# Kernel tuning notes

Measured on AMD Instinct MI355X. Metric: run time of the kernel, lower is better.

The kernel has to match this reference:

```python
import jax, jax.numpy as jnp
import numpy as np

QK_I2_S = 128  # elements per packed block (32 bytes -> 128 2-bit weights)


def unpack_weights_simd(packed):
    """Unpack SIMD block-interleaved 2-bit ternary weights.

    packed: (M, K//4) int values in [0, 256). Per 32-byte block, byte j holds
    weights at offsets j+0 (bits 6:7), j+32 (bits 4:5), j+64 (bits 2:3), j+96 (bits 0:1).
    Returns float32 (M, K) with values in {-1, 0, 1, 2}-1 = {-1,0,1,2}? (2-bit code minus 1).
    """
    M, Kp = packed.shape
    nb = Kp // 32                      # number of 128-element blocks
    p = packed.reshape(M, nb, 32)
    shifts = jnp.array([6, 4, 2, 0], dtype=jnp.int32)
    # (M, nb, 4, 32): axis 2 indexes the offset group {0,32,64,96}
    w = ((p[:, :, None, :] >> shifts[None, None, :, None]) & 3).astype(jnp.float32) - 1.0
    return w.reshape(M, nb * QK_I2_S)  # (M, K)


def quantize_activations_i8(x):
    """Per-token symmetric int8 quantization (absmax -> [-128, 127])."""
    absmax = jnp.max(jnp.abs(x), axis=-1, keepdims=True)
    q_scale = 127.0 / jnp.clip(absmax, 1e-5, None)   # x_i8 = round(x * q_scale)
    x_i8 = jnp.clip(jnp.round(x * q_scale), -128.0, 127.0)
    act_scale = 1.0 / q_scale                         # dequant scale = absmax/127
    return x_i8, act_scale


def setup_inputs() -> dict:
    key = jax.random.key(0)
    k1, k2, k3 = jax.random.split(key, 3)
    x = jax.random.normal(k1, (2, 2048, 4096), dtype=jnp.float32)
    weight = jax.random.randint(k2, (12288, 1024), 0, 256, dtype=jnp.int32)
    weight_scale = jax.random.uniform(k3, (1,), dtype=jnp.float32, minval=0.01, maxval=0.1)
    return {"x": x, "weight": weight, "weight_scale": weight_scale}


def reference(x, weight, weight_scale):
    orig_shape = x.shape[:-1]
    K = x.shape[-1]
    x_flat = x.reshape(-1, K).astype(jnp.float32)
    x_i8, act_scale = quantize_activations_i8(x_flat)      # (N,K), (N,1)
    W = unpack_weights_simd(weight)                         # (M,K) ternary-coded floats
    # bitnet_gemm: int8 activations x ternary weights, fused weight scale
    out = jnp.einsum('nk,mk->nm', x_i8, W) * weight_scale[0]
    out = (out * act_scale).astype(x.dtype)                 # dequantize activations
    return out.reshape(*orig_shape, -1)
```

## Files before the change

kernel.cpp:

```cpp
#include <hip/hip_runtime.h>

#define K_DIM 4096
#define M_DIM 12288
#define KW 1024
#define NT_K 32
#define BM 256
#define BN 256
#define GN 16
#define GM 48

typedef __attribute__((ext_vector_type(4))) int i32x4;
typedef __attribute__((ext_vector_type(16))) int i32x16;
typedef __attribute__((ext_vector_type(4))) unsigned int u32x4;
typedef __attribute__((ext_vector_type(4))) float f32x4;

__device__ __forceinline__ int quant1(float v, float qs) {
  float r = rintf(v * qs);
  r = fminf(127.f, fmaxf(-128.f, r));
  return (int)r;
}

__device__ __forceinline__ unsigned int unp(unsigned int uv) {
  return ((uv >> 6) | (uv << 4) | (uv << 14) | (uv << 24)) & 0x03030303u;
}

__global__ __launch_bounds__(256) void aux_kernel(const float* __restrict__ x,
                                                  const int* __restrict__ wp,
                                                  u32x4* __restrict__ xq2,
                                                  u32x4* __restrict__ wu2,
                                                  float2* __restrict__ scales) {
  __shared__ float redf[4];
  __shared__ int redi[4];
  __shared__ u32x4 ldsT[32][9];
  const int t = threadIdx.x;

  if (blockIdx.x < 4096) {
    const int n = blockIdx.x;
    const f32x4* __restrict__ row4 = (const f32x4*)(x + (size_t)n * K_DIM);

    float am = 0.f;
#pragma unroll
    for (int p = 0; p < 4; ++p) {
      f32x4 v = row4[t + 256 * p];
      am = fmaxf(am, fmaxf(fmaxf(fabsf(v[0]), fabsf(v[1])), fmaxf(fabsf(v[2]), fabsf(v[3]))));
    }
#pragma unroll
    for (int off = 32; off; off >>= 1) am = fmaxf(am, __shfl_xor(am, off, 64));
    const int wave = t >> 6, lane = t & 63;
    if (lane == 0) redf[wave] = am;
    __syncthreads();
    am = fmaxf(fmaxf(redf[0], redf[1]), fmaxf(redf[2], redf[3]));
    const float clipped = fmaxf(am, 1e-5f);
    const float qs = 127.0f / clipped;

    f32x4 v[4];
#pragma unroll
    for (int s = 0; s < 4; ++s) v[s] = row4[(t >> 3) * 32 + (t & 7) + 8 * s];
    unsigned int wds[4];
    int rsum = 0;
#pragma unroll
    for (int m = 0; m < 4; ++m) {
      const int q0 = quant1(v[0][m], qs);
      const int q1 = quant1(v[1][m], qs);
      const int q2 = quant1(v[2][m], qs);
      const int q3 = quant1(v[3][m], qs);
      rsum += q0 + q1 + q2 + q3;
      wds[m] = (unsigned int)(q0 & 255) | ((unsigned int)(q1 & 255) << 8) |
               ((unsigned int)(q2 & 255) << 16) | ((unsigned int)(q3 & 255) << 24);
    }
    xq2[(size_t)t * 4096 + n] = (u32x4){wds[0], wds[1], wds[2], wds[3]};

#pragma unroll
    for (int off = 32; off; off >>= 1) rsum += __shfl_xor(rsum, off, 64);
    if (lane == 0) redi[wave] = rsum;
    __syncthreads();
    if (t == 0)
      scales[n] = make_float2(clipped * (1.0f / 127.0f),
                              (float)(redi[0] + redi[1] + redi[2] + redi[3]));
  } else {
    const int bid = blockIdx.x - 4096;
    const int mt = bid >> 5, kb = bid & 31;
    const int m0 = mt * 256;
    const i32x4* __restrict__ in4 = (const i32x4*)wp;
#pragma unroll 2
    for (int it = 0; it < 8; ++it) {
      const int m = m0 + it * 32 + (t >> 3);
      const i32x4 vv = in4[(size_t)m * 256 + kb * 8 + (t & 7)];
      ldsT[t >> 3][t & 7] = (u32x4){unp((unsigned int)vv[0]), unp((unsigned int)vv[1]),
                                    unp((unsigned int)vv[2]), unp((unsigned int)vv[3])};
      __syncthreads();
      wu2[(size_t)(kb * 8 + (t >> 5)) * M_DIM + m0 + it * 32 + (t & 31)] = ldsT[t & 31][t >> 5];
      __syncthreads();
    }
  }
}

#define DSR(dst, addr, off) \
  asm volatile("ds_read_b128 %0, %1 offset:" #off : "=v"(dst) : "v"(addr))
#define LGKM(n) asm volatile("s_waitcnt lgkmcnt(" #n ")")

#define RD_KS0(s) { DSR(af[s][0], aA, 0);     DSR(af[s][1], aA, 512);   DSR(af[s][2], aA, 1024);  DSR(af[s][3], aA, 1536);  DSR(bf[s][0], bA, 0);     DSR(bf[s][1], bA, 512);   }
#define RD_KS1(s) { DSR(af[s][0], aA, 8192);  DSR(af[s][1], aA, 8704);  DSR(af[s][2], aA, 9216);  DSR(af[s][3], aA, 9728);  DSR(bf[s][0], bA, 8192);  DSR(bf[s][1], bA, 8704);  }
#define RD_KS2(s) { DSR(af[s][0], aA, 16384); DSR(af[s][1], aA, 16896); DSR(af[s][2], aA, 17408); DSR(af[s][3], aA, 17920); DSR(bf[s][0], bA, 16384); DSR(bf[s][1], bA, 16896); }
#define RD_KS3(s) { DSR(af[s][0], aA, 24576); DSR(af[s][1], aA, 25088); DSR(af[s][2], aA, 25600); DSR(af[s][3], aA, 26112); DSR(bf[s][0], bA, 24576); DSR(bf[s][1], bA, 25088); }

#define MFMA8(s)                                                                       \
  {                                                                                    \
    __builtin_amdgcn_s_setprio(1);                                                     \
    _Pragma("unroll") for (int i_ = 0; i_ < 4; ++i_)                                   \
        _Pragma("unroll") for (int j_ = 0; j_ < 2; ++j_) acc[i_][j_] =                 \
            __builtin_amdgcn_mfma_i32_32x32x32_i8(af[s][i_], bf[s][j_], acc[i_][j_],   \
                                                  0, 0, 0);                            \
    __builtin_amdgcn_s_setprio(0);                                                     \
  }

__global__ __launch_bounds__(512, 2) void bitgemm32(const unsigned char* __restrict__ xq2,
                                                    const unsigned char* __restrict__ wu2,
                                                    const float2* __restrict__ scales,
                                                    const float* __restrict__ wsp,
                                                    float* __restrict__ out) {
  __shared__ __align__(16) unsigned char lds[131072];

  const int tid = threadIdx.x;
  const int l = tid & 63;
  const int w = tid >> 6;
  const int wm = w >> 2;
  const int wn = w & 3;

  const int cpx = gridDim.x >> 3;
  const int swz = (blockIdx.x & 7) * cpx + (blockIdx.x >> 3);
  const int bn = swz & (GN - 1);
  const int bm = swz >> 4;

  const unsigned char* aBase =
      xq2 + ((size_t)(tid >> 8) * 4096 + (size_t)bn * 256 + (tid & 255)) * 16;
  const unsigned char* bBase =
      wu2 + ((size_t)(tid >> 8) * 12288 + (size_t)bm * 256 + (tid & 255)) * 16;
  const int ldsDst = tid * 16;

  const int aFB = (l >> 5) * 4096 + (wm * 128 + (l & 31)) * 16;
  const int bFB = (l >> 5) * 4096 + (wn * 64 + (l & 31)) * 16;
  const unsigned ldsBase = (unsigned)(size_t)lds;

  i32x16 acc[4][2];
#pragma unroll
  for (int i = 0; i < 4; ++i)
#pragma unroll
    for (int j = 0; j < 2; ++j)
#pragma unroll
      for (int r = 0; r < 16; ++r) acc[i][j][r] = 0;

  auto stage = [&](int buf, int kb) {
    unsigned char* ad = lds + buf * 32768 + ldsDst;
    unsigned char* bd = lds + 65536 + buf * 32768 + ldsDst;
    const unsigned char* as_ = aBase + (size_t)kb * 524288;
    const unsigned char* bs_ = bBase + (size_t)kb * 1572864;
#pragma unroll
    for (int q = 0; q < 4; ++q) {
      __builtin_amdgcn_global_load_lds(
          (const __attribute__((address_space(1))) void*)(as_ + (size_t)q * 131072),
          (__attribute__((address_space(3))) void*)(ad + q * 8192), 16, 0, 0);
      __builtin_amdgcn_global_load_lds(
          (const __attribute__((address_space(1))) void*)(bs_ + (size_t)q * 393216),
          (__attribute__((address_space(3))) void*)(bd + q * 8192), 16, 0, 0);
    }
  };

  i32x4 af[2][4], bf[2][4];

  stage(0, 0);
  for (int kb = 0; kb < NT_K; ++kb) {
    const int cur = kb & 1;
    if (kb + 1 < NT_K) {
      stage(cur ^ 1, kb + 1);
      asm volatile("s_waitcnt vmcnt(8)" ::: "memory");
    } else {
      asm volatile("s_waitcnt vmcnt(0)" ::: "memory");
    }
    __builtin_amdgcn_s_barrier();
    __builtin_amdgcn_sched_barrier(0);

    const unsigned aA = ldsBase + cur * 32768 + aFB;
    const unsigned bA = ldsBase + 65536 + cur * 32768 + bFB;

    RD_KS0(0);
    RD_KS1(1);
    LGKM(6);
    __builtin_amdgcn_sched_barrier(0);
    MFMA8(0);
    RD_KS2(0);
    LGKM(6);
    __builtin_amdgcn_sched_barrier(0);
    MFMA8(1);
    RD_KS3(1);
    LGKM(6);
    __builtin_amdgcn_sched_barrier(0);
    MFMA8(0);
    LGKM(0);
    __builtin_amdgcn_sched_barrier(0);
    MFMA8(1);
    __builtin_amdgcn_s_barrier();
  }

  const float wsc = wsp[0];
#pragma unroll
  for (int i = 0; i < 4; ++i) {
#pragma unroll
    for (int r = 0; r < 16; ++r) {
      const int n = bn * BM + wm * 128 + i * 32 + (r & 3) + 8 * (r >> 2) + 4 * (l >> 5);
      const float2 sc = scales[n];
      const float f = wsc * sc.x;
      float* orow = out + (size_t)n * M_DIM + bm * BN + wn * 64 + (l & 31);
#pragma unroll
      for (int j = 0; j < 2; ++j) orow[j * 32] = ((float)acc[i][j][r] - sc.y) * f;
    }
  }
}

extern "C" void kernel_launch(void* const* d_in, const int* in_sizes, int n_in,
                              void* d_out, int out_size, void* d_ws, size_t ws_size,
                              hipStream_t stream) {
  const float* x = (const float*)d_in[0];
  const int* wp = (const int*)d_in[1];
  const float* wsp = (const float*)d_in[2];
  float* out = (float*)d_out;
  const int N = in_sizes[0] / K_DIM;

  float2* scales = (float2*)d_ws;
  u32x4* xq2 = (u32x4*)((char*)d_ws + 32768);
  u32x4* wu2 = (u32x4*)((char*)d_ws + 32768 + (size_t)N * K_DIM);

  aux_kernel<<<4096 + 1536, 256, 0, stream>>>(x, wp, xq2, wu2, scales);
  const int grid = (N / BM) * GM;
  bitgemm32<<<grid, 512, 0, stream>>>((const unsigned char*)xq2, (const unsigned char*)wu2,
                                      scales, wsp, out);
}
```

Measured before the change: 236.3 us.

## Split next-tile prefetch into four phases interleaved with per-quarter MFMA blocks

The K-tile loop is restructured into four phases. Each phase issues one quarter of the next tile's global-to-LDS loads, reads one quarter of the current tile from LDS, and runs its MFMA block. This spreads global memory traffic across the iteration and cuts the fragment registers from double to single buffering. In exchange it adds a workgroup barrier around every phase and waits on all LDS reads before each MFMA group, which removes the overlap the previous double-buffered register pipeline had between LDS reads and MFMAs.

```diff
diff --git a/kernel.cpp b/kernel.cpp
--- a/kernel.cpp
+++ b/kernel.cpp
@@ -99,19 +99,43 @@
   asm volatile("ds_read_b128 %0, %1 offset:" #off : "=v"(dst) : "v"(addr))
 #define LGKM(n) asm volatile("s_waitcnt lgkmcnt(" #n ")")
 
-#define RD_KS0(s) { DSR(af[s][0], aA, 0);     DSR(af[s][1], aA, 512);   DSR(af[s][2], aA, 1024);  DSR(af[s][3], aA, 1536);  DSR(bf[s][0], bA, 0);     DSR(bf[s][1], bA, 512);   }
-#define RD_KS1(s) { DSR(af[s][0], aA, 8192);  DSR(af[s][1], aA, 8704);  DSR(af[s][2], aA, 9216);  DSR(af[s][3], aA, 9728);  DSR(bf[s][0], bA, 8192);  DSR(bf[s][1], bA, 8704);  }
-#define RD_KS2(s) { DSR(af[s][0], aA, 16384); DSR(af[s][1], aA, 16896); DSR(af[s][2], aA, 17408); DSR(af[s][3], aA, 17920); DSR(bf[s][0], bA, 16384); DSR(bf[s][1], bA, 16896); }
-#define RD_KS3(s) { DSR(af[s][0], aA, 24576); DSR(af[s][1], aA, 25088); DSR(af[s][2], aA, 25600); DSR(af[s][3], aA, 26112); DSR(bf[s][0], bA, 24576); DSR(bf[s][1], bA, 25088); }
-
-#define MFMA8(s)                                                                       \
+#define RD_Q0 { DSR(af[0], aA, 0);     DSR(af[1], aA, 512);   DSR(af[2], aA, 1024);  DSR(af[3], aA, 1536);  DSR(bf[0], bA, 0);     DSR(bf[1], bA, 512);   }
+#define RD_Q1 { DSR(af[0], aA, 8192);  DSR(af[1], aA, 8704);  DSR(af[2], aA, 9216);  DSR(af[3], aA, 9728);  DSR(bf[0], bA, 8192);  DSR(bf[1], bA, 8704);  }
+#define RD_Q2 { DSR(af[0], aA, 16384); DSR(af[1], aA, 16896); DSR(af[2], aA, 17408); DSR(af[3], aA, 17920); DSR(bf[0], bA, 16384); DSR(bf[1], bA, 16896); }
+#define RD_Q3 { DSR(af[0], aA, 24576); DSR(af[1], aA, 25088); DSR(af[2], aA, 25600); DSR(af[3], aA, 26112); DSR(bf[0], bA, 24576); DSR(bf[1], bA, 25088); }
+
+#define MFMA8                                                                          \
   {                                                                                    \
     __builtin_amdgcn_s_setprio(1);                                                     \
     _Pragma("unroll") for (int i_ = 0; i_ < 4; ++i_)                                   \
         _Pragma("unroll") for (int j_ = 0; j_ < 2; ++j_) acc[i_][j_] =                 \
-            __builtin_amdgcn_mfma_i32_32x32x32_i8(af[s][i_], bf[s][j_], acc[i_][j_],   \
+            __builtin_amdgcn_mfma_i32_32x32x32_i8(af[i_], bf[j_], acc[i_][j_],         \
                                                   0, 0, 0);                            \
     __builtin_amdgcn_s_setprio(0);                                                     \
+  }
+
+#define PHASE0(STG, WAITC)               \
+  {                                      \
+    STG;                                 \
+    WAITC;                               \
+    __builtin_amdgcn_s_barrier();        \
+    __builtin_amdgcn_sched_barrier(0);   \
+    RD_Q0;                               \
+    LGKM(0);                             \
+    __builtin_amdgcn_sched_barrier(0);   \
+    MFMA8;                               \
+    __builtin_amdgcn_s_barrier();        \
+  }
+
+#define PHASE(RD, STG)                   \
+  {                                      \
+    RD;                                  \
+    STG;                                 \
+    __builtin_amdgcn_s_barrier();        \
+    LGKM(0);                             \
+    __builtin_amdgcn_sched_barrier(0);   \
+    MFMA8;                               \
+    __builtin_amdgcn_s_barrier();        \
   }
 
 __global__ __launch_bounds__(512, 2) void bitgemm32(const unsigned char* __restrict__ xq2,
@@ -150,56 +174,42 @@
 #pragma unroll
       for (int r = 0; r < 16; ++r) acc[i][j][r] = 0;
 
-  auto stage = [&](int buf, int kb) {
-    unsigned char* ad = lds + buf * 32768 + ldsDst;
-    unsigned char* bd = lds + 65536 + buf * 32768 + ldsDst;
-    const unsigned char* as_ = aBase + (size_t)kb * 524288;
-    const unsigned char* bs_ = bBase + (size_t)kb * 1572864;
-#pragma unroll
-    for (int q = 0; q < 4; ++q) {
-      __builtin_amdgcn_global_load_lds(
-          (const __attribute__((address_space(1))) void*)(as_ + (size_t)q * 131072),
-          (__attribute__((address_space(3))) void*)(ad + q * 8192), 16, 0, 0);
-      __builtin_amdgcn_global_load_lds(
-          (const __attribute__((address_space(1))) void*)(bs_ + (size_t)q * 393216),
-          (__attribute__((address_space(3))) void*)(bd + q * 8192), 16, 0, 0);
-    }
+  auto stageQ = [&](int buf, int kb, int q) {
+    __builtin_amdgcn_global_load_lds(
+        (const __attribute__((address_space(1))) void*)(aBase + (size_t)kb * 524288 +
+                                                        (size_t)q * 131072),
+        (__attribute__((address_space(3))) void*)(lds + buf * 32768 + ldsDst + q * 8192), 16, 0,
+        0);
+    __builtin_amdgcn_global_load_lds(
+        (const __attribute__((address_space(1))) void*)(bBase + (size_t)kb * 1572864 +
+                                                        (size_t)q * 393216),
+        (__attribute__((address_space(3))) void*)(lds + 65536 + buf * 32768 + ldsDst + q * 8192),
+        16, 0, 0);
   };
 
-  i32x4 af[2][4], bf[2][4];
-
-  stage(0, 0);
+  i32x4 af[4], bf[2];
+
+#pragma unroll
+  for (int q = 0; q < 4; ++q) stageQ(0, 0, q);
+
   for (int kb = 0; kb < NT_K; ++kb) {
     const int cur = kb & 1;
-    if (kb + 1 < NT_K) {
-      stage(cur ^ 1, kb + 1);
-      asm volatile("s_waitcnt vmcnt(8)" ::: "memory");
-    } else {
-      asm volatile("s_waitcnt vmcnt(0)" ::: "memory");
-    }
-    __builtin_amdgcn_s_barrier();
-    __builtin_amdgcn_sched_barrier(0);
-
+    const int nbuf = cur ^ 1;
+    const bool pf = (kb + 1 < NT_K);
     const unsigned aA = ldsBase + cur * 32768 + aFB;
     const unsigned bA = ldsBase + 65536 + cur * 32768 + bFB;
 
-    RD_KS0(0);
-    RD_KS1(1);
-    LGKM(6);
-    __builtin_amdgcn_sched_barrier(0);
-    MFMA8(0);
-    RD_KS2(0);
-    LGKM(6);
-    __builtin_amdgcn_sched_barrier(0);
-    MFMA8(1);
-    RD_KS3(1);
-    LGKM(6);
-    __builtin_amdgcn_sched_barrier(0);
-    MFMA8(0);
-    LGKM(0);
-    __builtin_amdgcn_sched_barrier(0);
-    MFMA8(1);
-    __builtin_amdgcn_s_barrier();
+    if (pf) {
+      PHASE0(stageQ(nbuf, kb + 1, 0), asm volatile("s_waitcnt vmcnt(2)" ::: "memory"));
+      PHASE(RD_Q1, stageQ(nbuf, kb + 1, 1));
+      PHASE(RD_Q2, stageQ(nbuf, kb + 1, 2));
+      PHASE(RD_Q3, stageQ(nbuf, kb + 1, 3));
+    } else {
+      PHASE0(, asm volatile("s_waitcnt vmcnt(0)" ::: "memory"));
+      PHASE(RD_Q1, );
+      PHASE(RD_Q2, );
+      PHASE(RD_Q3, );
+    }
   }
 
   const float wsc = wsp[0];
```

Measured after the change: 230.3 us (median of 3 runs). 2.5% less time.

## Shrink GEMM tile to 256x128 with single-buffered LDS and 4-wave blocks

Applied to the files above, without the earlier changes.

The GEMM block tile drops from 256x256 with 8 waves to 256x128 with 4 waves, and the grid doubles to 1536 blocks. LDS shrinks from 128KB double-buffered to 48KB single-buffered, so each k-step waits for its own loads before computing. The aim is more resident blocks per CU and better load balance across the grid. The cost is losing the load/compute overlap inside a block and more total A-tile traffic, since each activation tile is now reloaded for twice as many M blocks.

```diff
diff --git a/kernel.cpp b/kernel.cpp
--- a/kernel.cpp
+++ b/kernel.cpp
@@ -2,12 +2,11 @@
 
 #define K_DIM 4096
 #define M_DIM 12288
-#define KW 1024
 #define NT_K 32
 #define BM 256
-#define BN 256
+#define BN 128
 #define GN 16
-#define GM 48
+#define GM2 96
 
 typedef __attribute__((ext_vector_type(4))) int i32x4;
 typedef __attribute__((ext_vector_type(16))) int i32x16;
@@ -98,11 +97,12 @@
 #define DSR(dst, addr, off) \
   asm volatile("ds_read_b128 %0, %1 offset:" #off : "=v"(dst) : "v"(addr))
 #define LGKM(n) asm volatile("s_waitcnt lgkmcnt(" #n ")")
+#define SB __builtin_amdgcn_sched_barrier(0)
 
 #define RD_KS0(s) { DSR(af[s][0], aA, 0);     DSR(af[s][1], aA, 512);   DSR(af[s][2], aA, 1024);  DSR(af[s][3], aA, 1536);  DSR(bf[s][0], bA, 0);     DSR(bf[s][1], bA, 512);   }
-#define RD_KS1(s) { DSR(af[s][0], aA, 8192);  DSR(af[s][1], aA, 8704);  DSR(af[s][2], aA, 9216);  DSR(af[s][3], aA, 9728);  DSR(bf[s][0], bA, 8192);  DSR(bf[s][1], bA, 8704);  }
-#define RD_KS2(s) { DSR(af[s][0], aA, 16384); DSR(af[s][1], aA, 16896); DSR(af[s][2], aA, 17408); DSR(af[s][3], aA, 17920); DSR(bf[s][0], bA, 16384); DSR(bf[s][1], bA, 16896); }
-#define RD_KS3(s) { DSR(af[s][0], aA, 24576); DSR(af[s][1], aA, 25088); DSR(af[s][2], aA, 25600); DSR(af[s][3], aA, 26112); DSR(bf[s][0], bA, 24576); DSR(bf[s][1], bA, 25088); }
+#define RD_KS1(s) { DSR(af[s][0], aA, 8192);  DSR(af[s][1], aA, 8704);  DSR(af[s][2], aA, 9216);  DSR(af[s][3], aA, 9728);  DSR(bf[s][0], bA, 4096);  DSR(bf[s][1], bA, 4608);  }
+#define RD_KS2(s) { DSR(af[s][0], aA, 16384); DSR(af[s][1], aA, 16896); DSR(af[s][2], aA, 17408); DSR(af[s][3], aA, 17920); DSR(bf[s][0], bA, 8192);  DSR(bf[s][1], bA, 8704);  }
+#define RD_KS3(s) { DSR(af[s][0], aA, 24576); DSR(af[s][1], aA, 25088); DSR(af[s][2], aA, 25600); DSR(af[s][3], aA, 26112); DSR(bf[s][0], bA, 12288); DSR(bf[s][1], bA, 12800); }
 
 #define MFMA8(s)                                                                       \
   {                                                                                    \
@@ -114,33 +114,35 @@
     __builtin_amdgcn_s_setprio(0);                                                     \
   }
 
-__global__ __launch_bounds__(512, 2) void bitgemm32(const unsigned char* __restrict__ xq2,
+__global__ __launch_bounds__(256, 2) void bitgemm3b(const unsigned char* __restrict__ xq2,
                                                     const unsigned char* __restrict__ wu2,
                                                     const float2* __restrict__ scales,
                                                     const float* __restrict__ wsp,
                                                     float* __restrict__ out) {
-  __shared__ __align__(16) unsigned char lds[131072];
+  __shared__ __align__(16) unsigned char lds[49152];
 
   const int tid = threadIdx.x;
   const int l = tid & 63;
   const int w = tid >> 6;
-  const int wm = w >> 2;
-  const int wn = w & 3;
+  const int wm = w >> 1;
+  const int wn = w & 1;
 
   const int cpx = gridDim.x >> 3;
   const int swz = (blockIdx.x & 7) * cpx + (blockIdx.x >> 3);
   const int bn = swz & (GN - 1);
   const int bm = swz >> 4;
 
-  const unsigned char* aBase =
-      xq2 + ((size_t)(tid >> 8) * 4096 + (size_t)bn * 256 + (tid & 255)) * 16;
+  const unsigned char* aBase = xq2 + ((size_t)bn * 256 + tid) * 16;
+  const int ldsDstA = tid * 16;
   const unsigned char* bBase =
-      wu2 + ((size_t)(tid >> 8) * 12288 + (size_t)bm * 256 + (tid & 255)) * 16;
-  const int ldsDst = tid * 16;
+      wu2 + ((size_t)(tid >> 7) * M_DIM + (size_t)bm * 128 + (tid & 127)) * 16;
+  const int ldsDstB = 32768 + (tid >> 7) * 2048 + (tid & 127) * 16;
 
   const int aFB = (l >> 5) * 4096 + (wm * 128 + (l & 31)) * 16;
-  const int bFB = (l >> 5) * 4096 + (wn * 64 + (l & 31)) * 16;
+  const int bFB = (l >> 5) * 2048 + (wn * 64 + (l & 31)) * 16;
   const unsigned ldsBase = (unsigned)(size_t)lds;
+  const unsigned aA = ldsBase + aFB;
+  const unsigned bA = ldsBase + 32768 + bFB;
 
   i32x16 acc[4][2];
 #pragma unroll
@@ -150,56 +152,45 @@
 #pragma unroll
       for (int r = 0; r < 16; ++r) acc[i][j][r] = 0;
 
-  auto stage = [&](int buf, int kb) {
-    unsigned char* ad = lds + buf * 32768 + ldsDst;
-    unsigned char* bd = lds + 65536 + buf * 32768 + ldsDst;
+  auto stage = [&](int kb) {
     const unsigned char* as_ = aBase + (size_t)kb * 524288;
     const unsigned char* bs_ = bBase + (size_t)kb * 1572864;
-#pragma unroll
-    for (int q = 0; q < 4; ++q) {
+    unsigned char* ad = lds + ldsDstA;
+    unsigned char* bd = lds + ldsDstB;
+#pragma unroll
+    for (int q = 0; q < 8; ++q)
       __builtin_amdgcn_global_load_lds(
-          (const __attribute__((address_space(1))) void*)(as_ + (size_t)q * 131072),
-          (__attribute__((address_space(3))) void*)(ad + q * 8192), 16, 0, 0);
+          (const __attribute__((address_space(1))) void*)(as_ + (size_t)q * 65536),
+          (__attribute__((address_space(3))) void*)(ad + q * 4096), 16, 0, 0);
+#pragma unroll
+    for (int q = 0; q < 4; ++q)
       __builtin_amdgcn_global_load_lds(
           (const __attribute__((address_space(1))) void*)(bs_ + (size_t)q * 393216),
-          (__attribute__((address_space(3))) void*)(bd + q * 8192), 16, 0, 0);
-    }
+          (__attribute__((address_space(3))) void*)(bd + q * 4096), 16, 0, 0);
   };
 
-  i32x4 af[2][4], bf[2][4];
-
-  stage(0, 0);
+  i32x4 af[2][4], bf[2][2];
+
   for (int kb = 0; kb < NT_K; ++kb) {
-    const int cur = kb & 1;
-    if (kb + 1 < NT_K) {
-      stage(cur ^ 1, kb + 1);
-      asm volatile("s_waitcnt vmcnt(8)" ::: "memory");
-    } else {
-      asm volatile("s_waitcnt vmcnt(0)" ::: "memory");
-    }
+    stage(kb);
+    asm volatile("s_waitcnt vmcnt(0)" ::: "memory");
     __builtin_amdgcn_s_barrier();
-    __builtin_amdgcn_sched_barrier(0);
-
-    const unsigned aA = ldsBase + cur * 32768 + aFB;
-    const unsigned bA = ldsBase + 65536 + cur * 32768 + bFB;
+    SB;
 
     RD_KS0(0);
     RD_KS1(1);
-    LGKM(6);
-    __builtin_amdgcn_sched_barrier(0);
+    LGKM(6); SB;
     MFMA8(0);
     RD_KS2(0);
-    LGKM(6);
-    __builtin_amdgcn_sched_barrier(0);
+    LGKM(6); SB;
     MFMA8(1);
     RD_KS3(1);
-    LGKM(6);
-    __builtin_amdgcn_sched_barrier(0);
+    LGKM(6); SB;
     MFMA8(0);
-    LGKM(0);
-    __builtin_amdgcn_sched_barrier(0);
+    LGKM(0); SB;
     MFMA8(1);
     __builtin_amdgcn_s_barrier();
+    SB;
   }
 
   const float wsc = wsp[0];
@@ -231,7 +222,7 @@
   u32x4* wu2 = (u32x4*)((char*)d_ws + 32768 + (size_t)N * K_DIM);
 
   aux_kernel<<<4096 + 1536, 256, 0, stream>>>(x, wp, xq2, wu2, scales);
-  const int grid = (N / BM) * GM;
-  bitgemm32<<<grid, 512, 0, stream>>>((const unsigned char*)xq2, (const unsigned char*)wu2,
+  const int grid = GN * GM2;
+  bitgemm3b<<<grid, 256, 0, stream>>>((const unsigned char*)xq2, (const unsigned char*)wu2,
                                       scales, wsp, out);
 }
```

Result: slower. 248.4 us (+5.1%).
